# Kernel tuning notes

Hardware: AMD Instinct MI355X
Metric: run time of the kernel (lower is better)

Reference implementation:

```python
import jax, jax.numpy as jnp
import numpy as np

V = 32000      # vocab
TMAX = 1024    # BLOCK_SIZE
D = 768        # N_EMBD
H = 12         # N_HEAD
L = 12         # N_LAYER
HS = D // H    # head_size
FF = 4 * D
B, T = 4, 1024


def setup_inputs() -> dict:
    key = jax.random.key(0)
    ks = iter(jax.random.split(key, 40))
    n = lambda shape: 0.02 * jax.random.normal(next(ks), shape, dtype=jnp.float32)
    return dict(
        idx=jax.random.randint(next(ks), (B, T), 0, V),
        targets=jax.random.randint(next(ks), (B, T), 0, V),
        tok_emb=n((V, D)),
        pos_emb=n((TMAX, D)),
        Wq=n((L, H, D, HS)), Wk=n((L, H, D, HS)), Wv=n((L, H, D, HS)),
        Wo=n((L, D, D)), bo=jnp.zeros((L, D)),
        W1=n((L, D, FF)), b1=jnp.zeros((L, FF)),
        W2=n((L, FF, D)), b2=jnp.zeros((L, D)),
        ln1_g=jnp.ones((L, D)), ln1_b=jnp.zeros((L, D)),
        ln2_g=jnp.ones((L, D)), ln2_b=jnp.zeros((L, D)),
        lnf_g=jnp.ones((D,)), lnf_b=jnp.zeros((D,)),
        Wlm=n((D, V)), blm=jnp.zeros((V,)),
    )


def _ln(x, g, b, eps=1e-5):
    m = x.mean(-1, keepdims=True)
    v = x.var(-1, keepdims=True)
    return (x - m) * jax.lax.rsqrt(v + eps) * g + b


def reference(idx, targets, tok_emb, pos_emb, Wq, Wk, Wv, Wo, bo,
              W1, b1, W2, b2, ln1_g, ln1_b, ln2_g, ln2_b, lnf_g, lnf_b,
              Wlm, blm):
    Bsz, Tt = idx.shape
    x = tok_emb[idx] + pos_emb[:Tt]                      # [B,T,D]
    causal = jnp.tril(jnp.ones((Tt, Tt), dtype=bool))     # [T,T]

    def layer(x, p):
        wq, wk, wv, wo, bob, w1, b1b, w2, b2b, g1, be1, g2, be2 = p
        h = _ln(x, g1, be1)
        q = jnp.einsum('btd,hdk->bhtk', h, wq)
        k = jnp.einsum('btd,hdk->bhtk', h, wk)
        v = jnp.einsum('btd,hdk->bhtk', h, wv)
        wei = jnp.einsum('bhtk,bhsk->bhts', q, k) * (HS ** -0.5)
        wei = jnp.where(causal, wei, -jnp.inf)
        wei = jax.nn.softmax(wei, axis=-1)                # dropout=0 in eval
        att = jnp.einsum('bhts,bhsk->bhtk', wei, v)
        att = att.transpose(0, 2, 1, 3).reshape(Bsz, Tt, H * HS)  # concat heads
        x = x + att @ wo + bob
        h2 = _ln(x, g2, be2)
        x = x + jax.nn.relu(h2 @ w1 + b1b) @ w2 + b2b
        return x, None

    x, _ = jax.lax.scan(layer, x,
                        (Wq, Wk, Wv, Wo, bo, W1, b1, W2, b2,
                         ln1_g, ln1_b, ln2_g, ln2_b))
    x = _ln(x, lnf_g, lnf_b)
    logits = x @ Wlm + blm                                # [B,T,V]
    lf = logits.reshape(Bsz * Tt, V)
    tf = targets.reshape(-1)
    logp = jax.nn.log_softmax(lf, axis=-1)
    loss = -jnp.take_along_axis(logp, tf[:, None], axis=1).mean()
    return lf, loss
```

## Files before the change

### kernel.cpp

```cpp
#include <hip/hip_runtime.h>

constexpr int C_B   = 4;
constexpr int C_T   = 1024;
constexpr int C_D   = 768;
constexpr int C_H   = 12;
constexpr int C_HS  = 64;
constexpr int C_FF  = 3072;
constexpr int C_V   = 32000;
constexpr int C_L   = 12;
constexpr int ROWS  = C_B * C_T;
constexpr int QKVN  = 3 * C_D;
constexpr int NCB   = C_V / 256;

typedef __bf16 bf16;
typedef __attribute__((ext_vector_type(8))) __bf16 bf16x8;
typedef __attribute__((ext_vector_type(4))) float  f32x4;
typedef __attribute__((ext_vector_type(4))) short  s16x4;

static __device__ __forceinline__ void gload16(const void* g, void* l) {
  __builtin_amdgcn_global_load_lds((const __attribute__((address_space(1))) void*)g,
                                   (__attribute__((address_space(3))) void*)l,
                                   16, 0, 0);
}

__global__ __launch_bounds__(256) void embed_kernel(const int* __restrict__ idx,
    const float* __restrict__ tok, const float* __restrict__ pos, float* __restrict__ x) {
  int gid = blockIdx.x * 256 + threadIdx.x;
  int row = gid / C_D, d = gid - row * C_D;
  int t = row & (C_T - 1);
  x[gid] = tok[(long)idx[row] * C_D + d] + pos[(long)t * C_D + d];
}

__global__ __launch_bounds__(256) void ln_kernel(const float* __restrict__ x,
    const float* __restrict__ g, const float* __restrict__ bb, long goff,
    bf16* __restrict__ out) {
  int row = blockIdx.x, tid = threadIdx.x;
  const float* xr = x + (long)row * C_D;
  float v0 = xr[tid], v1 = xr[tid + 256], v2 = xr[tid + 512];
  float s = v0 + v1 + v2;
  float s2 = v0 * v0 + v1 * v1 + v2 * v2;
#pragma unroll
  for (int off = 32; off > 0; off >>= 1) {
    s  += __shfl_down(s, off);
    s2 += __shfl_down(s2, off);
  }
  __shared__ float sm[4], sq[4];
  if ((tid & 63) == 0) { sm[tid >> 6] = s; sq[tid >> 6] = s2; }
  __syncthreads();
  s  = sm[0] + sm[1] + sm[2] + sm[3];
  s2 = sq[0] + sq[1] + sq[2] + sq[3];
  float mean = s * (1.f / C_D);
  float var  = s2 * (1.f / C_D) - mean * mean;
  float rstd = rsqrtf(var + 1e-5f);
  bf16* orow = out + (long)row * C_D;
  orow[tid]       = (bf16)((v0 - mean) * rstd * g[goff + tid]       + bb[goff + tid]);
  orow[tid + 256] = (bf16)((v1 - mean) * rstd * g[goff + tid + 256] + bb[goff + tid + 256]);
  orow[tid + 512] = (bf16)((v2 - mean) * rstd * g[goff + tid + 512] + bb[goff + tid + 512]);
}

__global__ __launch_bounds__(256) void transpose_kernel(const float* __restrict__ src,
    bf16* __restrict__ dst, int K, int N, long soff0, int ntn) {
  __shared__ bf16 tile[32][33];
  const float* s = src + soff0;
  int tn = blockIdx.x % ntn, tk = blockIdx.x / ntn;
  int c = threadIdx.x & 31, r = threadIdx.x >> 5;
#pragma unroll
  for (int it = 0; it < 4; ++it)
    tile[r + 8 * it][c] = (bf16)s[(long)(tk * 32 + r + 8 * it) * N + tn * 32 + c];
  __syncthreads();
#pragma unroll
  for (int it = 0; it < 4; ++it)
    dst[(long)(tn * 32 + r + 8 * it) * K + tk * 32 + c] = tile[c][r + 8 * it];
}

__global__ __launch_bounds__(256) void transpose_layer_kernel(
    const float* __restrict__ Wq, const float* __restrict__ Wk,
    const float* __restrict__ Wv, const float* __restrict__ Wo,
    const float* __restrict__ W1, const float* __restrict__ W2,
    bf16* __restrict__ wqkvt, bf16* __restrict__ wot,
    bf16* __restrict__ w1t, bf16* __restrict__ w2t, int l) {
  int bid = blockIdx.x;
  const float* src; bf16* dst; int K, N, ntn, t;
  if (bid < 1728) {
    int which = bid / 576, r = bid % 576, head = r / 48;
    t = r % 48;
    const float* W = which == 0 ? Wq : which == 1 ? Wk : Wv;
    src = W + (long)l * C_H * C_D * C_HS + (long)head * C_D * C_HS;
    dst = wqkvt + (long)which * C_D * C_D + (long)head * C_HS * C_D;
    K = C_D; N = C_HS; ntn = 2;
  } else if (bid < 2304) {
    t = bid - 1728; src = Wo + (long)l * C_D * C_D; dst = wot;
    K = C_D; N = C_D; ntn = 24;
  } else if (bid < 4608) {
    t = bid - 2304; src = W1 + (long)l * C_D * C_FF; dst = w1t;
    K = C_D; N = C_FF; ntn = 96;
  } else {
    t = bid - 4608; src = W2 + (long)l * C_FF * C_D; dst = w2t;
    K = C_FF; N = C_D; ntn = 24;
  }
  __shared__ bf16 tile[32][33];
  int tn = t % ntn, tk = t / ntn;
  int c = threadIdx.x & 31, r = threadIdx.x >> 5;
#pragma unroll
  for (int it = 0; it < 4; ++it)
    tile[r + 8 * it][c] = (bf16)src[(long)(tk * 32 + r + 8 * it) * N + tn * 32 + c];
  __syncthreads();
#pragma unroll
  for (int it = 0; it < 4; ++it)
    dst[(long)(tn * 32 + r + 8 * it) * K + tk * 32 + c] = tile[c][r + 8 * it];
}

template <int MODE>
__global__ __launch_bounds__(512) void gemm256(const bf16* __restrict__ A,
    const bf16* __restrict__ Bt, const float* __restrict__ bias, long boff,
    void* __restrict__ outp, float* __restrict__ lossp, int N, int K) {
  __shared__ __attribute__((aligned(16))) char smem[131072];
  int tid = threadIdx.x;
  int l = tid & 63, w = tid >> 6;
  int wm = w >> 2, wn = w & 3;
  int lg = l >> 4, lr = l & 15;

  int nwg = gridDim.x;
  int fid = blockIdx.x;
  int swz = (fid & 7) * (nwg >> 3) + (fid >> 3);
  long row0 = (long)(swz & 15) * 256;
  long col0 = (long)(swz >> 4) * 256;
  int cbi = (int)(col0 >> 8);

  int Y0 = tid * 16, Y1 = 8192 + tid * 16;
  auto dec = [](int Y, int& R, int& C) {
    int s = Y >> 10, y = Y & 1023;
    int r15 = y >> 6, z = y & 63;
    int q = (z ^ ((r15 & 8) << 2)) >> 4;
    R = (s >> 1) * 16 + r15;
    C = (s & 1) * 32 + q * 8;
  };
  int R0, C0, R1, C1;
  dec(Y0, R0, C0);  dec(Y1, R1, C1);
  const bf16* Ab = A  + row0 * K;
  const bf16* Bb = Bt + col0 * K;

  auto stage = [&](int d, int kt) {
    char* bb = smem + d * 65536;
    long kc = (long)kt * 64;
    gload16(Ab + (long)R0 * K + kc + C0, bb + Y0);
    gload16(Ab + (long)R1 * K + kc + C1, bb + Y1);
    gload16(Ab + (long)(128 + R0) * K + kc + C0, bb + 16384 + Y0);
    gload16(Ab + (long)(128 + R1) * K + kc + C1, bb + 16384 + Y1);
    gload16(Bb + (long)R0 * K + kc + C0, bb + 32768 + Y0);
    gload16(Bb + (long)R1 * K + kc + C1, bb + 32768 + Y1);
    gload16(Bb + (long)(128 + R0) * K + kc + C0, bb + 49152 + Y0);
    gload16(Bb + (long)(128 + R1) * K + kc + C1, bb + 49152 + Y1);
  };

  f32x4 acc[8][4];
  const f32x4 fz = {0.f, 0.f, 0.f, 0.f};
#pragma unroll
  for (int mf = 0; mf < 8; ++mf)
#pragma unroll
    for (int nf = 0; nf < 4; ++nf) acc[mf][nf] = fz;

  int aoff = lr * 64 + ((lg * 16) ^ ((lr & 8) << 2));
  int nk = K >> 6;
  stage(0, 0);
  int d = 0;
  for (int kt = 0; kt < nk; ++kt) {
    __syncthreads();
    if (kt + 1 < nk) stage(d ^ 1, kt + 1);
    const char* aB = smem + d * 65536 + wm * 16384;
    const char* bB = smem + d * 65536 + 32768 + (wn >> 1) * 16384;
    bf16x8 bfrag[4][2];
#pragma unroll
    for (int nf = 0; nf < 4; ++nf)
#pragma unroll
      for (int k = 0; k < 2; ++k)
        bfrag[nf][k] = *(const bf16x8*)(bB + ((((wn & 1) * 4 + nf) * 2 + k) << 10) + aoff);
#pragma unroll
    for (int p = 0; p < 4; ++p) {
      bf16x8 af[2][2];
#pragma unroll
      for (int mi = 0; mi < 2; ++mi)
#pragma unroll
        for (int k = 0; k < 2; ++k)
          af[mi][k] = *(const bf16x8*)(aB + (((p * 2 + mi) * 2 + k) << 10) + aoff);
      __builtin_amdgcn_s_setprio(1);
#pragma unroll
      for (int mi = 0; mi < 2; ++mi)
#pragma unroll
        for (int nf = 0; nf < 4; ++nf)
#pragma unroll
          for (int k = 0; k < 2; ++k)
            acc[p * 2 + mi][nf] = __builtin_amdgcn_mfma_f32_16x16x32_bf16(
                af[mi][k], bfrag[nf][k], acc[p * 2 + mi][nf], 0, 0, 0);
      __builtin_amdgcn_s_setprio(0);
    }
    d ^= 1;
  }
  __syncthreads();

#pragma unroll
  for (int h = 0; h < 2; ++h) {
    if (h) __syncthreads();
    if (wm == h) {
      float* lf = (float*)smem;
#pragma unroll
      for (int nf = 0; nf < 4; ++nf) {
        int col = wn * 64 + nf * 16 + lr;
        float bv = bias ? bias[boff + col0 + col] : 0.f;
#pragma unroll
        for (int mf = 0; mf < 8; ++mf) {
          int rb = mf * 16 + lg * 4;
#pragma unroll
          for (int r = 0; r < 4; ++r)
            lf[(rb + r) * 256 + col] = acc[mf][nf][r] + bv;
        }
      }
    }
    __syncthreads();
#pragma unroll
    for (int it = 0; it < 16; ++it) {
      int byte = it * 8192 + tid * 16;
      int rl = byte >> 10, cb = byte & 1023;
      *(f32x4*)((float*)outp + (row0 + h * 128 + rl) * N + col0 + (cb >> 2)) =
          *(const f32x4*)(smem + byte);
    }
    if (lossp) {
      const float* lf = (const float*)smem;
      int row = tid >> 2, chunk = tid & 3;
      float M = -1e30f, S = 0.f;
#pragma unroll
      for (int j = 0; j < 16; ++j) {
        int jj = (j + row) & 15;
        f32x4 v = *(const f32x4*)(lf + row * 256 + chunk * 64 + jj * 4);
#pragma unroll
        for (int q = 0; q < 4; ++q) {
          float xv = v[q];
          if (xv > M) { S *= __expf(M - xv); M = xv; }
          S += __expf(xv - M);
        }
      }
#pragma unroll
      for (int off = 1; off < 4; off <<= 1) {
        float Mo = __shfl_xor(M, off), So = __shfl_xor(S, off);
        float Mn = fmaxf(M, Mo);
        S = S * __expf(M - Mn) + So * __expf(Mo - Mn);
        M = Mn;
      }
      if (chunk == 0) {
        long pi = ((row0 + h * 128 + row) * NCB + cbi) * 2;
        lossp[pi] = M;  lossp[pi + 1] = S;
      }
    }
  }
}

template <int MODE>
__global__ __launch_bounds__(256) void gemm_bt(const bf16* __restrict__ A,
    const bf16* __restrict__ Bt, const float* __restrict__ bias, long boff,
    void* __restrict__ outp, float* __restrict__ resid, int N, int K) {
  __shared__ __attribute__((aligned(16))) char smem[32768];
  int tid = threadIdx.x;
  int l = tid & 63;
  int w = tid >> 6, wr = w >> 1, wc = w & 1;
  int lg = l >> 4, lr = l & 15;

  int nwg = gridDim.x;
  int fid = blockIdx.x;
  int swz = (fid & 7) * (nwg >> 3) + (fid >> 3);
  long row0 = (long)(swz & 31) * 128;
  long col0 = (long)(swz >> 5) * 128;

  const bf16* ga = A  + (row0 + (tid >> 2)) * K + (tid & 3) * 8;
  const bf16* gb = Bt + (col0 + (tid >> 2)) * K + (tid & 3) * 8;

  f32x4 acc[4][4];
  const f32x4 fz = {0.f, 0.f, 0.f, 0.f};
#pragma unroll
  for (int m = 0; m < 4; ++m)
#pragma unroll
    for (int n = 0; n < 4; ++n) acc[m][n] = fz;

  int nk = K >> 5;
  {
    bf16* la = (bf16*)smem + tid * 8;
    bf16* lb = (bf16*)(smem + 8192) + tid * 8;
    gload16(ga, la);  gload16(ga + (long)64 * K, la + 2048);
    gload16(gb, lb);  gload16(gb + (long)64 * K, lb + 2048);
    ga += 32; gb += 32;
  }
  int cur = 0;
  for (int t = 0; t < nk; ++t) {
    __syncthreads();
    if (t + 1 < nk) {
      char* bufb = smem + (cur ^ 1) * 16384;
      bf16* la = (bf16*)bufb + tid * 8;
      bf16* lb = (bf16*)(bufb + 8192) + tid * 8;
      gload16(ga, la);  gload16(ga + (long)64 * K, la + 2048);
      gload16(gb, lb);  gload16(gb + (long)64 * K, lb + 2048);
      ga += 32; gb += 32;
    }
    const bf16* cA = (const bf16*)(smem + cur * 16384);
    const bf16* cB = (const bf16*)(smem + cur * 16384 + 8192);
    bf16x8 af[4], bfr[4];
#pragma unroll
    for (int m = 0; m < 4; ++m)
      af[m] = *(const bf16x8*)(cA + (wr * 64 + m * 16 + lr) * 32 + lg * 8);
#pragma unroll
    for (int n = 0; n < 4; ++n)
      bfr[n] = *(const bf16x8*)(cB + (wc * 64 + n * 16 + lr) * 32 + lg * 8);
#pragma unroll
    for (int m = 0; m < 4; ++m)
#pragma unroll
      for (int n = 0; n < 4; ++n)
        acc[m][n] = __builtin_amdgcn_mfma_f32_16x16x32_bf16(af[m], bfr[n], acc[m][n], 0, 0, 0);
    cur ^= 1;
  }
  __syncthreads();

  if (MODE == 0 || MODE == 1) {
    bf16* lc = (bf16*)smem;
#pragma unroll
    for (int n = 0; n < 4; ++n) {
      int gcl = wc * 64 + n * 16 + lr;
      float bv = bias ? bias[boff + col0 + gcl] : 0.f;
#pragma unroll
      for (int m = 0; m < 4; ++m) {
        int rb = wr * 64 + m * 16 + lg * 4;
#pragma unroll
        for (int r = 0; r < 4; ++r) {
          float v = acc[m][n][r] + bv;
          if (MODE == 1) v = fmaxf(v, 0.f);
          lc[(rb + r) * 128 + gcl] = (bf16)v;
        }
      }
    }
    __syncthreads();
#pragma unroll
    for (int it = 0; it < 8; ++it) {
      int byte = it * 4096 + tid * 16;
      int rl = byte >> 8;
      int cb = byte & 255;
      *(bf16x8*)((bf16*)outp + (row0 + rl) * N + col0 + (cb >> 1)) =
          *(const bf16x8*)(smem + byte);
    }
  } else {
#pragma unroll
    for (int pair = 0; pair < 2; ++pair) {
      float* lcf = (float*)smem;
#pragma unroll
      for (int n = 0; n < 4; ++n) {
        int gcl = wc * 64 + n * 16 + lr;
        float bv = bias ? bias[boff + col0 + gcl] : 0.f;
#pragma unroll
        for (int mi = 0; mi < 2; ++mi) {
          int m = pair * 2 + mi;
          int rl = wr * 32 + mi * 16 + lg * 4;
#pragma unroll
          for (int r = 0; r < 4; ++r)
            lcf[(rl + r) * 128 + gcl] = acc[m][n][r] + bv;
        }
      }
      __syncthreads();
#pragma unroll
      for (int it = 0; it < 8; ++it) {
        int byte = it * 4096 + tid * 16;
        int rl = byte >> 9;
        int cb = byte & 511;
        long gr = row0 + (rl >> 5) * 64 + pair * 32 + ((rl >> 4) & 1) * 16 + (rl & 15);
        f32x4 v = *(const f32x4*)(smem + byte);
        f32x4 g = *(const f32x4*)(resid + gr * N + col0 + (cb >> 2));
        v += g;
        *(f32x4*)(resid + gr * N + col0 + (cb >> 2)) = v;
      }
      __syncthreads();
    }
  }
}

#define TRRD(D, OFF) asm volatile("ds_read_b64_tr_b16 %0, %1 offset:" OFF \
                                  : "=v"(D) : "v"(trp))
__global__ __launch_bounds__(64) void attn_kernel(const bf16* __restrict__ qkv,
                                                  bf16* __restrict__ attout) {
  int fid = blockIdx.x;
  int swzb = (fid & 7) * 384 + (fid >> 3);
  int qt = swzb & 63;
  int bh = swzb >> 6;
  int b = bh / C_H, h = bh % C_H;
  int l = threadIdx.x;
  int lg = l >> 4, lr = l & 15;
  const bf16* base = qkv + (long)b * C_T * QKVN;

  const bf16* qp = base + (long)(qt * 16 + lr) * QKVN + h * C_HS;
  bf16x8 qf0 = *(const bf16x8*)(qp + lg * 8);
  bf16x8 qf1 = *(const bf16x8*)(qp + 32 + lg * 8);

  const f32x4 fz = {0.f, 0.f, 0.f, 0.f};
  f32x4 o[4] = {fz, fz, fz, fz};
  float m_run[4], l_run[4];
#pragma unroll
  for (int r = 0; r < 4; ++r) { m_run[r] = -1e30f; l_run[r] = 0.f; }

  __shared__ __attribute__((aligned(16))) bf16 p_lds[16][80];
  __shared__ __attribute__((aligned(16))) bf16 vt_sub[4096];

  unsigned trp = (unsigned)(unsigned long)
      ((const __attribute__((address_space(3))) char*)vt_sub + l * 8);

  int nkt = (qt * 16 + 15) / 64 + 1;
  for (int kt = 0; kt < nkt; ++kt) {
    int key0 = kt * 64;
    f32x4 sacc[4];
#pragma unroll
    for (int ss = 0; ss < 4; ++ss) {
      const bf16* kp = base + (long)(key0 + ss * 16 + lr) * QKVN + C_D + h * C_HS;
      bf16x8 kf0 = *(const bf16x8*)(kp + lg * 8);
      bf16x8 kf1 = *(const bf16x8*)(kp + 32 + lg * 8);
      f32x4 a = fz;
      a = __builtin_amdgcn_mfma_f32_16x16x32_bf16(qf0, kf0, a, 0, 0, 0);
      a = __builtin_amdgcn_mfma_f32_16x16x32_bf16(qf1, kf1, a, 0, 0, 0);
      sacc[ss] = a;
    }
#pragma unroll
    for (int r = 0; r < 4; ++r) {
      int qrow = qt * 16 + lg * 4 + r;
      float sv[4];
#pragma unroll
      for (int ss = 0; ss < 4; ++ss) {
        bool u = (key0 + ss * 16 + lr) <= qrow;
        sv[ss] = u ? sacc[ss][r] * 0.125f : -1e30f;
      }
      float mr = fmaxf(fmaxf(sv[0], sv[1]), fmaxf(sv[2], sv[3]));
      mr = fmaxf(mr, __shfl_xor(mr, 1));
      mr = fmaxf(mr, __shfl_xor(mr, 2));
      mr = fmaxf(mr, __shfl_xor(mr, 4));
      mr = fmaxf(mr, __shfl_xor(mr, 8));
      float mnew = fmaxf(m_run[r], mr);
      float scale = __expf(m_run[r] - mnew);
      float pv[4], rs = 0.f;
#pragma unroll
      for (int ss = 0; ss < 4; ++ss) {
        pv[ss] = sv[ss] > -1e29f ? __expf(sv[ss] - mnew) : 0.f;
        rs += pv[ss];
      }
      rs += __shfl_xor(rs, 1);
      rs += __shfl_xor(rs, 2);
      rs += __shfl_xor(rs, 4);
      rs += __shfl_xor(rs, 8);
      l_run[r] = l_run[r] * scale + rs;
      m_run[r] = mnew;
      o[0][r] *= scale; o[1][r] *= scale; o[2][r] *= scale; o[3][r] *= scale;
#pragma unroll
      for (int ss = 0; ss < 4; ++ss)
        p_lds[lg * 4 + r][ss * 16 + lr] = (bf16)pv[ss];
    }
#pragma unroll
    for (int it = 0; it < 8; ++it) {
      int kl = it * 8 + (l >> 3);
      int d0 = (l & 7) * 8;
      bf16x8 vv = *(const bf16x8*)(base + (long)(key0 + kl) * QKVN + 2 * C_D + h * C_HS + d0);
      int klh = kl & 31;
      int ba = ((kl >> 5) << 12) + ((d0 >> 4) << 10) + (((klh >> 2) & 1) << 9)
             + ((klh >> 3) << 7) + ((klh & 3) << 5) + ((d0 & 15) << 1);
      *(bf16x8*)((char*)vt_sub + ba) = vv;
    }
    __syncthreads();
    s16x4 h0[8], h1[8];
    TRRD(h0[0], "0");    TRRD(h0[1], "512");
    TRRD(h0[2], "1024"); TRRD(h0[3], "1536");
    TRRD(h0[4], "2048"); TRRD(h0[5], "2560");
    TRRD(h0[6], "3072"); TRRD(h0[7], "3584");
    TRRD(h1[0], "4096"); TRRD(h1[1], "4608");
    TRRD(h1[2], "5120"); TRRD(h1[3], "5632");
    TRRD(h1[4], "6144"); TRRD(h1[5], "6656");
    TRRD(h1[6], "7168"); TRRD(h1[7], "7680");
    bf16x8 pf0 = *(const bf16x8*)(&p_lds[lr][lg * 8]);
    bf16x8 pf1 = *(const bf16x8*)(&p_lds[lr][32 + lg * 8]);
    asm volatile("s_waitcnt lgkmcnt(0)" ::: "memory");
    __builtin_amdgcn_sched_barrier(0);
    union uu { short s[8]; bf16x8 v; };
    auto mk = [](s16x4 a, s16x4 bq) {
      uu u;
      u.s[0] = a[0]; u.s[1] = a[1]; u.s[2] = a[2]; u.s[3] = a[3];
      u.s[4] = bq[0]; u.s[5] = bq[1]; u.s[6] = bq[2]; u.s[7] = bq[3];
      return u.v;
    };
#pragma unroll
    for (int c = 0; c < 4; ++c) {
      o[c] = __builtin_amdgcn_mfma_f32_16x16x32_bf16(pf0, mk(h0[c*2], h0[c*2+1]), o[c], 0, 0, 0);
      o[c] = __builtin_amdgcn_mfma_f32_16x16x32_bf16(pf1, mk(h1[c*2], h1[c*2+1]), o[c], 0, 0, 0);
    }
    __syncthreads();
  }
#pragma unroll
  for (int c = 0; c < 4; ++c)
#pragma unroll
    for (int r = 0; r < 4; ++r) {
      int qrow = qt * 16 + lg * 4 + r;
      attout[((long)b * C_T + qrow) * C_D + h * C_HS + c * 16 + lr] =
          (bf16)(o[c][r] / l_run[r]);
    }
}

__global__ __launch_bounds__(128) void loss_partial_kernel(const float* __restrict__ lossp,
    const float* __restrict__ logits, const int* __restrict__ targets,
    float* __restrict__ rowloss) {
  int row = blockIdx.x * 128 + threadIdx.x;
  const float* pp = lossp + (long)row * NCB * 2;
  float M = -1e30f, S = 0.f;
  for (int i = 0; i < NCB; ++i) {
    float pm = pp[i * 2], ps = pp[i * 2 + 1];
    float Mn = fmaxf(M, pm);
    S = S * __expf(M - Mn) + ps * __expf(pm - Mn);
    M = Mn;
  }
  float lt = logits[(long)row * C_V + targets[row]];
  rowloss[row] = -(lt - M - logf(S));
}

__global__ __launch_bounds__(256) void loss_final(const float* __restrict__ rowloss,
                                                  float* __restrict__ out) {
  int tid = threadIdx.x;
  float s = 0.f;
  for (int i = tid; i < ROWS; i += 256) s += rowloss[i];
#pragma unroll
  for (int off = 32; off > 0; off >>= 1) s += __shfl_down(s, off);
  __shared__ float sm[4];
  if ((tid & 63) == 0) sm[tid >> 6] = s;
  __syncthreads();
  if (tid == 0) out[0] = (sm[0] + sm[1] + sm[2] + sm[3]) * (1.f / ROWS);
}

extern "C" void kernel_launch(void* const* d_in, const int* in_sizes, int n_in,
                              void* d_out, int out_size, void* d_ws, size_t ws_size,
                              hipStream_t stream) {
  (void)in_sizes; (void)n_in; (void)out_size; (void)ws_size;
  const int*   idx     = (const int*)  d_in[0];
  const int*   targets = (const int*)  d_in[1];
  const float* tok     = (const float*)d_in[2];
  const float* pos     = (const float*)d_in[3];
  const float* Wq      = (const float*)d_in[4];
  const float* Wk      = (const float*)d_in[5];
  const float* Wv      = (const float*)d_in[6];
  const float* Wo      = (const float*)d_in[7];
  const float* bo      = (const float*)d_in[8];
  const float* W1      = (const float*)d_in[9];
  const float* b1      = (const float*)d_in[10];
  const float* W2      = (const float*)d_in[11];
  const float* b2      = (const float*)d_in[12];
  const float* ln1g    = (const float*)d_in[13];
  const float* ln1b    = (const float*)d_in[14];
  const float* ln2g    = (const float*)d_in[15];
  const float* ln2b    = (const float*)d_in[16];
  const float* lnfg    = (const float*)d_in[17];
  const float* lnfb    = (const float*)d_in[18];
  const float* Wlm     = (const float*)d_in[19];
  const float* blm     = (const float*)d_in[20];

  char* p = (char*)d_ws;
  auto alloc = [&](size_t bytes) {
    char* r = p; p += (bytes + 255) & ~(size_t)255; return r;
  };
  float* x       = (float*)alloc((size_t)ROWS * C_D * 4);
  bf16*  h       = (bf16*) alloc((size_t)ROWS * C_D * 2);
  bf16*  qkv     = (bf16*) alloc((size_t)ROWS * QKVN * 2);
  bf16*  attout  = (bf16*) alloc((size_t)ROWS * C_D * 2);
  bf16*  ffbuf   = (bf16*) alloc((size_t)ROWS * C_FF * 2);
  bf16*  wqkvt   = (bf16*) alloc((size_t)QKVN * C_D * 2);
  bf16*  wot     = (bf16*) alloc((size_t)C_D * C_D * 2);
  bf16*  w1t     = (bf16*) alloc((size_t)C_FF * C_D * 2);
  bf16*  w2t     = (bf16*) alloc((size_t)C_D * C_FF * 2);
  float* rowloss = (float*)alloc((size_t)ROWS * 4);
  float* lossp   = (float*)alloc((size_t)ROWS * NCB * 2 * 4);
  bf16*  wlmt    = qkv;

  float* logits = (float*)d_out;

  embed_kernel<<<ROWS * C_D / 256, 256, 0, stream>>>(idx, tok, pos, x);

  for (int l = 0; l < C_L; ++l) {
    transpose_layer_kernel<<<6912, 256, 0, stream>>>(
        Wq, Wk, Wv, Wo, W1, W2, wqkvt, wot, w1t, w2t, l);

    ln_kernel<<<ROWS, 256, 0, stream>>>(x, ln1g, ln1b, (long)l * C_D, h);
    gemm_bt<0><<<(QKVN / 128) * 32, 256, 0, stream>>>(
        h, wqkvt, nullptr, 0, qkv, nullptr, QKVN, C_D);
    attn_kernel<<<C_B * C_H * (C_T / 16), 64, 0, stream>>>(qkv, attout);
    gemm_bt<2><<<(C_D / 128) * 32, 256, 0, stream>>>(
        attout, wot, bo, (long)l * C_D, nullptr, x, C_D, C_D);
    ln_kernel<<<ROWS, 256, 0, stream>>>(x, ln2g, ln2b, (long)l * C_D, h);
    gemm_bt<1><<<(C_FF / 128) * 32, 256, 0, stream>>>(
        h, w1t, b1, (long)l * C_FF, ffbuf, nullptr, C_FF, C_D);
    gemm_bt<2><<<(C_D / 128) * 32, 256, 0, stream>>>(
        ffbuf, w2t, b2, (long)l * C_D, nullptr, x, C_D, C_FF);
  }

  transpose_kernel<<<(C_V / 32) * (C_D / 32), 256, 0, stream>>>(
      Wlm, wlmt, C_D, C_V, 0, C_V / 32);

  ln_kernel<<<ROWS, 256, 0, stream>>>(x, lnfg, lnfb, 0, h);
  gemm256<3><<<16 * (C_V / 256), 512, 0, stream>>>(
      h, wlmt, blm, 0, logits, lossp, C_V, C_D);
  loss_partial_kernel<<<ROWS / 128, 128, 0, stream>>>(lossp, logits, targets, rowloss);
  loss_final<<<1, 256, 0, stream>>>(rowloss, logits + (long)ROWS * C_V);
}
```

Measured before the change: 3.243 ms.

## Shrink attention key tile to 32 and interleave gemm256 warp row mapping

The attention kernel now walks keys in 32-key tiles instead of 64. For a 16-row query tile this cuts the fully masked work on the diagonal tile, and it halves the LDS used per block, which may allow more resident blocks. The trade-off is twice as many loop iterations, each with its own pair of __syncthreads. Separately, the LM-head gemm256 gives each warp row a 64-row strided slice rather than a contiguous 128-row half. Every warp therefore takes part in both epilogue phases, which spreads the LDS writes across all warps, and the unused MODE template parameter is removed.

```diff
diff --git a/kernel.cpp b/kernel.cpp
--- a/kernel.cpp
+++ b/kernel.cpp
@@ -110,10 +110,9 @@
     dst[(long)(tn * 32 + r + 8 * it) * K + tk * 32 + c] = tile[c][r + 8 * it];
 }
 
-template <int MODE>
 __global__ __launch_bounds__(512) void gemm256(const bf16* __restrict__ A,
     const bf16* __restrict__ Bt, const float* __restrict__ bias, long boff,
-    void* __restrict__ outp, float* __restrict__ lossp, int N, int K) {
+    float* __restrict__ outp, float* __restrict__ lossp, int N, int K) {
   __shared__ __attribute__((aligned(16))) char smem[131072];
   int tid = threadIdx.x;
   int l = tid & 63, w = tid >> 6;
@@ -167,7 +166,6 @@
   for (int kt = 0; kt < nk; ++kt) {
     __syncthreads();
     if (kt + 1 < nk) stage(d ^ 1, kt + 1);
-    const char* aB = smem + d * 65536 + wm * 16384;
     const char* bB = smem + d * 65536 + 32768 + (wn >> 1) * 16384;
     bf16x8 bfrag[4][2];
 #pragma unroll
@@ -181,8 +179,11 @@
 #pragma unroll
       for (int mi = 0; mi < 2; ++mi)
 #pragma unroll
-        for (int k = 0; k < 2; ++k)
-          af[mi][k] = *(const bf16x8*)(aB + (((p * 2 + mi) * 2 + k) << 10) + aoff);
+        for (int k = 0; k < 2; ++k) {
+          int f = p * 2 + mi;
+          const char* aB = smem + d * 65536 + (f >> 2) * 16384;
+          af[mi][k] = *(const bf16x8*)(aB + (((wm * 4 + (f & 3)) * 2 + k) << 10) + aoff);
+        }
       __builtin_amdgcn_s_setprio(1);
 #pragma unroll
       for (int mi = 0; mi < 2; ++mi)
@@ -201,19 +202,18 @@
 #pragma unroll
   for (int h = 0; h < 2; ++h) {
     if (h) __syncthreads();
-    if (wm == h) {
-      float* lf = (float*)smem;
+    float* lf = (float*)smem;
+#pragma unroll
+    for (int fq = 0; fq < 4; ++fq) {
+      int f = h * 4 + fq;
+      int rl = wm * 64 + fq * 16 + lg * 4;
 #pragma unroll
       for (int nf = 0; nf < 4; ++nf) {
         int col = wn * 64 + nf * 16 + lr;
         float bv = bias ? bias[boff + col0 + col] : 0.f;
 #pragma unroll
-        for (int mf = 0; mf < 8; ++mf) {
-          int rb = mf * 16 + lg * 4;
-#pragma unroll
-          for (int r = 0; r < 4; ++r)
-            lf[(rb + r) * 256 + col] = acc[mf][nf][r] + bv;
-        }
+        for (int r = 0; r < 4; ++r)
+          lf[(rl + r) * 256 + col] = acc[f][nf][r] + bv;
       }
     }
     __syncthreads();
@@ -221,17 +221,17 @@
     for (int it = 0; it < 16; ++it) {
       int byte = it * 8192 + tid * 16;
       int rl = byte >> 10, cb = byte & 1023;
-      *(f32x4*)((float*)outp + (row0 + h * 128 + rl) * N + col0 + (cb >> 2)) =
+      *(f32x4*)(outp + (row0 + h * 128 + rl) * N + col0 + (cb >> 2)) =
           *(const f32x4*)(smem + byte);
     }
     if (lossp) {
-      const float* lf = (const float*)smem;
+      const float* lfc = (const float*)smem;
       int row = tid >> 2, chunk = tid & 3;
       float M = -1e30f, S = 0.f;
 #pragma unroll
       for (int j = 0; j < 16; ++j) {
         int jj = (j + row) & 15;
-        f32x4 v = *(const f32x4*)(lf + row * 256 + chunk * 64 + jj * 4);
+        f32x4 v = *(const f32x4*)(lfc + row * 256 + chunk * 64 + jj * 4);
 #pragma unroll
         for (int q = 0; q < 4; ++q) {
           float xv = v[q];
@@ -400,18 +400,18 @@
 #pragma unroll
   for (int r = 0; r < 4; ++r) { m_run[r] = -1e30f; l_run[r] = 0.f; }
 
-  __shared__ __attribute__((aligned(16))) bf16 p_lds[16][80];
-  __shared__ __attribute__((aligned(16))) bf16 vt_sub[4096];
+  __shared__ __attribute__((aligned(16))) bf16 p_lds[16][40];
+  __shared__ __attribute__((aligned(16))) bf16 vt_sub[2048];
 
   unsigned trp = (unsigned)(unsigned long)
       ((const __attribute__((address_space(3))) char*)vt_sub + l * 8);
 
-  int nkt = (qt * 16 + 15) / 64 + 1;
+  int nkt = (qt * 16 + 15) / 32 + 1;
   for (int kt = 0; kt < nkt; ++kt) {
-    int key0 = kt * 64;
-    f32x4 sacc[4];
-#pragma unroll
-    for (int ss = 0; ss < 4; ++ss) {
+    int key0 = kt * 32;
+    f32x4 sacc[2];
+#pragma unroll
+    for (int ss = 0; ss < 2; ++ss) {
       const bf16* kp = base + (long)(key0 + ss * 16 + lr) * QKVN + C_D + h * C_HS;
       bf16x8 kf0 = *(const bf16x8*)(kp + lg * 8);
       bf16x8 kf1 = *(const bf16x8*)(kp + 32 + lg * 8);
@@ -423,25 +423,20 @@
 #pragma unroll
     for (int r = 0; r < 4; ++r) {
       int qrow = qt * 16 + lg * 4 + r;
-      float sv[4];
-#pragma unroll
-      for (int ss = 0; ss < 4; ++ss) {
-        bool u = (key0 + ss * 16 + lr) <= qrow;
-        sv[ss] = u ? sacc[ss][r] * 0.125f : -1e30f;
-      }
-      float mr = fmaxf(fmaxf(sv[0], sv[1]), fmaxf(sv[2], sv[3]));
+      bool u0 = (key0 + lr) <= qrow;
+      bool u1 = (key0 + 16 + lr) <= qrow;
+      float s0 = u0 ? sacc[0][r] * 0.125f : -1e30f;
+      float s1 = u1 ? sacc[1][r] * 0.125f : -1e30f;
+      float mr = fmaxf(s0, s1);
       mr = fmaxf(mr, __shfl_xor(mr, 1));
       mr = fmaxf(mr, __shfl_xor(mr, 2));
       mr = fmaxf(mr, __shfl_xor(mr, 4));
       mr = fmaxf(mr, __shfl_xor(mr, 8));
       float mnew = fmaxf(m_run[r], mr);
       float scale = __expf(m_run[r] - mnew);
-      float pv[4], rs = 0.f;
-#pragma unroll
-      for (int ss = 0; ss < 4; ++ss) {
-        pv[ss] = sv[ss] > -1e29f ? __expf(sv[ss] - mnew) : 0.f;
-        rs += pv[ss];
-      }
+      float p0 = u0 ? __expf(s0 - mnew) : 0.f;
+      float p1 = u1 ? __expf(s1 - mnew) : 0.f;
+      float rs = p0 + p1;
       rs += __shfl_xor(rs, 1);
       rs += __shfl_xor(rs, 2);
       rs += __shfl_xor(rs, 4);
@@ -449,32 +444,25 @@
       l_run[r] = l_run[r] * scale + rs;
       m_run[r] = mnew;
       o[0][r] *= scale; o[1][r] *= scale; o[2][r] *= scale; o[3][r] *= scale;
-#pragma unroll
-      for (int ss = 0; ss < 4; ++ss)
-        p_lds[lg * 4 + r][ss * 16 + lr] = (bf16)pv[ss];
-    }
-#pragma unroll
-    for (int it = 0; it < 8; ++it) {
+      p_lds[lg * 4 + r][lr]      = (bf16)p0;
+      p_lds[lg * 4 + r][16 + lr] = (bf16)p1;
+    }
+#pragma unroll
+    for (int it = 0; it < 4; ++it) {
       int kl = it * 8 + (l >> 3);
       int d0 = (l & 7) * 8;
       bf16x8 vv = *(const bf16x8*)(base + (long)(key0 + kl) * QKVN + 2 * C_D + h * C_HS + d0);
-      int klh = kl & 31;
-      int ba = ((kl >> 5) << 12) + ((d0 >> 4) << 10) + (((klh >> 2) & 1) << 9)
-             + ((klh >> 3) << 7) + ((klh & 3) << 5) + ((d0 & 15) << 1);
+      int ba = ((d0 >> 4) << 10) + (((kl >> 2) & 1) << 9) + ((kl >> 3) << 7)
+             + ((kl & 3) << 5) + ((d0 & 15) << 1);
       *(bf16x8*)((char*)vt_sub + ba) = vv;
     }
     __syncthreads();
-    s16x4 h0[8], h1[8];
-    TRRD(h0[0], "0");    TRRD(h0[1], "512");
-    TRRD(h0[2], "1024"); TRRD(h0[3], "1536");
-    TRRD(h0[4], "2048"); TRRD(h0[5], "2560");
-    TRRD(h0[6], "3072"); TRRD(h0[7], "3584");
-    TRRD(h1[0], "4096"); TRRD(h1[1], "4608");
-    TRRD(h1[2], "5120"); TRRD(h1[3], "5632");
-    TRRD(h1[4], "6144"); TRRD(h1[5], "6656");
-    TRRD(h1[6], "7168"); TRRD(h1[7], "7680");
-    bf16x8 pf0 = *(const bf16x8*)(&p_lds[lr][lg * 8]);
-    bf16x8 pf1 = *(const bf16x8*)(&p_lds[lr][32 + lg * 8]);
+    s16x4 t0a, t0b, t1a, t1b, t2a, t2b, t3a, t3b;
+    TRRD(t0a, "0");    TRRD(t0b, "512");
+    TRRD(t1a, "1024"); TRRD(t1b, "1536");
+    TRRD(t2a, "2048"); TRRD(t2b, "2560");
+    TRRD(t3a, "3072"); TRRD(t3b, "3584");
+    bf16x8 pf = *(const bf16x8*)(&p_lds[lr][lg * 8]);
     asm volatile("s_waitcnt lgkmcnt(0)" ::: "memory");
     __builtin_amdgcn_sched_barrier(0);
     union uu { short s[8]; bf16x8 v; };
@@ -484,11 +472,10 @@
       u.s[4] = bq[0]; u.s[5] = bq[1]; u.s[6] = bq[2]; u.s[7] = bq[3];
       return u.v;
     };
-#pragma unroll
-    for (int c = 0; c < 4; ++c) {
-      o[c] = __builtin_amdgcn_mfma_f32_16x16x32_bf16(pf0, mk(h0[c*2], h0[c*2+1]), o[c], 0, 0, 0);
-      o[c] = __builtin_amdgcn_mfma_f32_16x16x32_bf16(pf1, mk(h1[c*2], h1[c*2+1]), o[c], 0, 0, 0);
-    }
+    o[0] = __builtin_amdgcn_mfma_f32_16x16x32_bf16(pf, mk(t0a, t0b), o[0], 0, 0, 0);
+    o[1] = __builtin_amdgcn_mfma_f32_16x16x32_bf16(pf, mk(t1a, t1b), o[1], 0, 0, 0);
+    o[2] = __builtin_amdgcn_mfma_f32_16x16x32_bf16(pf, mk(t2a, t2b), o[2], 0, 0, 0);
+    o[3] = __builtin_amdgcn_mfma_f32_16x16x32_bf16(pf, mk(t3a, t3b), o[3], 0, 0, 0);
     __syncthreads();
   }
 #pragma unroll
@@ -598,7 +585,7 @@
       Wlm, wlmt, C_D, C_V, 0, C_V / 32);
 
   ln_kernel<<<ROWS, 256, 0, stream>>>(x, lnfg, lnfb, 0, h);
-  gemm256<3><<<16 * (C_V / 256), 512, 0, stream>>>(
+  gemm256<<<16 * (C_V / 256), 512, 0, stream>>>(
       h, wlmt, blm, 0, logits, lossp, C_V, C_D);
   loss_partial_kernel<<<ROWS / 128, 128, 0, stream>>>(lossp, logits, targets, rowloss);
   loss_final<<<1, 256, 0, stream>>>(rowloss, logits + (long)ROWS * C_V);
```

After: 2.981 ms. 1.09x faster.
